# Kernel tuning notes

Hardware: AMD Instinct MI355X
Metric: run time of the kernel (lower is better)

## Reference

```python
import jax, jax.numpy as jnp
import numpy as np

BN_EPS = 1e-5

def conv_block(x, w, b, g, beta, m, v, a):
    # 1x1 conv (pointwise) + eval-mode BatchNorm2d + PReLU (single shared alpha)
    y = jnp.einsum('oc,bcft->boft', w, x) + b[None, :, None, None]
    scale = (g / jnp.sqrt(v + BN_EPS))[None, :, None, None]
    y = (y - m[None, :, None, None]) * scale + beta[None, :, None, None]
    return jnp.where(y >= 0, y, a * y)

def setup_inputs() -> dict:
    key = jax.random.key(0)
    ks = jax.random.split(key, 16)
    B, C, F, T = 4, 64, 128, 512
    d_c = C // 2
    inp = jax.random.normal(ks[0], (B, C, F, T), dtype=jnp.float32)
    # qkv projection Conv2Dblock params (1x1 conv c -> d_c)
    w1 = jax.random.normal(ks[1], (d_c, C), dtype=jnp.float32) * (1.0 / np.sqrt(C))
    b1 = jax.random.normal(ks[2], (d_c,), dtype=jnp.float32) * 0.01
    g1 = jnp.ones((d_c,), jnp.float32)
    be1 = jnp.zeros((d_c,), jnp.float32)
    m1 = jax.random.normal(ks[3], (d_c,), dtype=jnp.float32) * 0.01
    v1 = jax.random.uniform(ks[4], (d_c,), jnp.float32, 0.5, 1.5)
    a1 = jnp.asarray(0.25, jnp.float32)
    # output projection Conv2Dblock params (1x1 conv d_c -> c)
    wp = jax.random.normal(ks[5], (C, d_c), dtype=jnp.float32) * (1.0 / np.sqrt(d_c))
    bp = jax.random.normal(ks[6], (C,), dtype=jnp.float32) * 0.01
    g2 = jnp.ones((C,), jnp.float32)
    be2 = jnp.zeros((C,), jnp.float32)
    m2 = jax.random.normal(ks[7], (C,), dtype=jnp.float32) * 0.01
    v2 = jax.random.uniform(ks[8], (C,), jnp.float32, 0.5, 1.5)
    a2 = jnp.asarray(0.25, jnp.float32)
    return {"inp": inp, "w1": w1, "b1": b1, "g1": g1, "be1": be1, "m1": m1,
            "v1": v1, "a1": a1, "wp": wp, "bp": bp, "g2": g2, "be2": be2,
            "m2": m2, "v2": v2, "a2": a2}

def reference(inp, w1, b1, g1, be1, m1, v1, a1, wp, bp, g2, be2, m2, v2, a2):
    d_c = w1.shape[0]
    qkv = conv_block(inp, w1, b1, g1, be1, m1, v1, a1)           # [B, d_c, F, T]
    # per-frequency time attention scores, then recombine with values
    score = jnp.einsum('bcft,bcfy->bfty', qkv, qkv) / jnp.sqrt(jnp.asarray(d_c, qkv.dtype))
    score = jnp.einsum('bfty,bcfy->bcft', score, qkv)            # [B, d_c, F, T]
    # causal mask applied over the last two dims (F, T), as in the original
    Fd, Td = score.shape[-2], score.shape[-1]
    mask = (jnp.arange(Td)[None, :] - jnp.arange(Fd)[:, None]) >= (Td - Fd + 1)
    neg = -jnp.finfo(score.dtype).max
    score = jnp.where(mask[None, None, :, :], neg, score)
    score = jax.nn.softmax(score, axis=-1)
    score = conv_block(score, wp, bp, g2, be2, m2, v2, a2)       # [B, C, F, T]
    return score + inp
```

## Files before the change

kernel.cpp:

```cpp
#include <hip/hip_runtime.h>
#include <math.h>

#define Bv  4
#define Cv  64
#define DCv 32
#define Fv  128
#define Tv  512
#define FT  (Fv * 512)

__global__ __launch_bounds__(512)
void kprep(const float* __restrict__ w1, const float* __restrict__ b1,
           const float* __restrict__ g1, const float* __restrict__ be1,
           const float* __restrict__ m1, const float* __restrict__ v1,
           const float* __restrict__ wp, const float* __restrict__ bp,
           const float* __restrict__ g2, const float* __restrict__ be2,
           const float* __restrict__ m2, const float* __restrict__ v2,
           float* __restrict__ W1T, float* __restrict__ B1f,
           float* __restrict__ W2f, float* __restrict__ B2f)
{
    const int tid = threadIdx.x;
    #pragma unroll
    for (int i = 0; i < 4; ++i) {
        const int e = tid * 4 + i;
        const int c = e & 31, k = e >> 5;
        W1T[e] = w1[c * Cv + k] * (g1[c] * rsqrtf(v1[c] + 1e-5f));
    }
    {
        const int o = tid >> 3;
        const float s = g2[o] * rsqrtf(v2[o] + 1e-5f);
        float4 v = *(const float4*)&wp[tid * 4];
        v.x *= s; v.y *= s; v.z *= s; v.w *= s;
        *(float4*)&W2f[tid * 4] = v;
    }
    if (tid < DCv) {
        const float s = g1[tid] * rsqrtf(v1[tid] + 1e-5f);
        B1f[tid] = (b1[tid] - m1[tid]) * s + be1[tid];
    }
    if (tid < Cv) {
        const float s = g2[tid] * rsqrtf(v2[tid] + 1e-5f);
        B2f[tid] = (bp[tid] - m2[tid]) * s + be2[tid];
    }
}

__global__ __launch_bounds__(256, 4)
void kc1_conv(const float* __restrict__ inp,
              const float* __restrict__ W1T, const float* __restrict__ B1f,
              const float* __restrict__ a1,
              float* __restrict__ Qws)
{
    __shared__ __align__(16) float sW[Cv * DCv];
    __shared__ float sB[DCv];

    const int tid = threadIdx.x;
    const int bid = blockIdx.x;
    const int h   = bid & 1;
    const int bf  = bid >> 1;
    const int b   = bf >> 7;
    const int f   = bf & 127;

    {
        const int e = tid * 8;
        *(float4*)&sW[e]     = *(const float4*)&W1T[e];
        *(float4*)&sW[e + 4] = *(const float4*)&W1T[e + 4];
    }
    if (tid < DCv) sB[tid] = B1f[tid];
    const float alpha1 = a1[0];
    __syncthreads();

    const int w  = tid >> 6, l = tid & 63;
    const int tl = l & 15, cl = l >> 4;
    const int r0 = cl * 8;
    const int t0 = h * 256 + w * 64 + tl * 4;

    const float* px = inp + (size_t)(b * Cv) * FT + f * 512 + t0;

    float acc[32];
    #pragma unroll
    for (int i = 0; i < 32; ++i) acc[i] = 0.f;

    #pragma unroll 8
    for (int k = 0; k < Cv; ++k) {
        const float4 x   = *(const float4*)&px[(size_t)k * FT];
        const float4 a0  = *(const float4*)&sW[k * DCv + r0];
        const float4 a1v = *(const float4*)&sW[k * DCv + r0 + 4];
        acc[0*4+0] = fmaf(a0.x, x.x, acc[0*4+0]); acc[0*4+1] = fmaf(a0.x, x.y, acc[0*4+1]);
        acc[0*4+2] = fmaf(a0.x, x.z, acc[0*4+2]); acc[0*4+3] = fmaf(a0.x, x.w, acc[0*4+3]);
        acc[1*4+0] = fmaf(a0.y, x.x, acc[1*4+0]); acc[1*4+1] = fmaf(a0.y, x.y, acc[1*4+1]);
        acc[1*4+2] = fmaf(a0.y, x.z, acc[1*4+2]); acc[1*4+3] = fmaf(a0.y, x.w, acc[1*4+3]);
        acc[2*4+0] = fmaf(a0.z, x.x, acc[2*4+0]); acc[2*4+1] = fmaf(a0.z, x.y, acc[2*4+1]);
        acc[2*4+2] = fmaf(a0.z, x.z, acc[2*4+2]); acc[2*4+3] = fmaf(a0.z, x.w, acc[2*4+3]);
        acc[3*4+0] = fmaf(a0.w, x.x, acc[3*4+0]); acc[3*4+1] = fmaf(a0.w, x.y, acc[3*4+1]);
        acc[3*4+2] = fmaf(a0.w, x.z, acc[3*4+2]); acc[3*4+3] = fmaf(a0.w, x.w, acc[3*4+3]);
        acc[4*4+0] = fmaf(a1v.x, x.x, acc[4*4+0]); acc[4*4+1] = fmaf(a1v.x, x.y, acc[4*4+1]);
        acc[4*4+2] = fmaf(a1v.x, x.z, acc[4*4+2]); acc[4*4+3] = fmaf(a1v.x, x.w, acc[4*4+3]);
        acc[5*4+0] = fmaf(a1v.y, x.x, acc[5*4+0]); acc[5*4+1] = fmaf(a1v.y, x.y, acc[5*4+1]);
        acc[5*4+2] = fmaf(a1v.y, x.z, acc[5*4+2]); acc[5*4+3] = fmaf(a1v.y, x.w, acc[5*4+3]);
        acc[6*4+0] = fmaf(a1v.z, x.x, acc[6*4+0]); acc[6*4+1] = fmaf(a1v.z, x.y, acc[6*4+1]);
        acc[6*4+2] = fmaf(a1v.z, x.z, acc[6*4+2]); acc[6*4+3] = fmaf(a1v.z, x.w, acc[6*4+3]);
        acc[7*4+0] = fmaf(a1v.w, x.x, acc[7*4+0]); acc[7*4+1] = fmaf(a1v.w, x.y, acc[7*4+1]);
        acc[7*4+2] = fmaf(a1v.w, x.z, acc[7*4+2]); acc[7*4+3] = fmaf(a1v.w, x.w, acc[7*4+3]);
    }

    const float b0 = sB[r0+0], b1_ = sB[r0+1], b2 = sB[r0+2], b3 = sB[r0+3];
    const float b4 = sB[r0+4], b5  = sB[r0+5], b6 = sB[r0+6], b7 = sB[r0+7];
    #pragma unroll
    for (int j = 0; j < 4; ++j) {
        float z0 = acc[0*4+j] + b0, z1 = acc[1*4+j] + b1_;
        float z2 = acc[2*4+j] + b2, z3 = acc[3*4+j] + b3;
        float z4 = acc[4*4+j] + b4, z5 = acc[5*4+j] + b5;
        float z6 = acc[6*4+j] + b6, z7 = acc[7*4+j] + b7;
        z0 = z0 >= 0.f ? z0 : alpha1 * z0;  z1 = z1 >= 0.f ? z1 : alpha1 * z1;
        z2 = z2 >= 0.f ? z2 : alpha1 * z2;  z3 = z3 >= 0.f ? z3 : alpha1 * z3;
        z4 = z4 >= 0.f ? z4 : alpha1 * z4;  z5 = z5 >= 0.f ? z5 : alpha1 * z5;
        z6 = z6 >= 0.f ? z6 : alpha1 * z6;  z7 = z7 >= 0.f ? z7 : alpha1 * z7;
        float4 v0; v0.x = z0; v0.y = z1; v0.z = z2; v0.w = z3;
        float4 v1; v1.x = z4; v1.y = z5; v1.z = z6; v1.w = z7;
        float* qg = Qws + ((size_t)bf * Tv + t0 + j) * DCv + r0;
        *(float4*)&qg[0] = v0;
        *(float4*)&qg[4] = v1;
    }
}

__global__ __launch_bounds__(256)
void km_build(const float* __restrict__ Qws, float* __restrict__ Mfull)
{
    __shared__ __align__(16) float sP[4][1024];

    const int tid   = threadIdx.x;
    const int bf    = blockIdx.x;
    const int slice = tid >> 6;
    const int l     = tid & 63;
    const int c1b   = l >> 3;
    const int c2b   = l & 7;

    const float* qp = Qws + ((size_t)bf * Tv + slice * 128) * DCv;
    float4 r0 = {0,0,0,0}, r1 = {0,0,0,0}, r2 = {0,0,0,0}, r3 = {0,0,0,0};
    #pragma unroll 4
    for (int i = 0; i < 128; ++i) {
        const float4 qa = *(const float4*)&qp[i * 32 + c1b * 4];
        const float4 qb = *(const float4*)&qp[i * 32 + c2b * 4];
        r0.x = fmaf(qa.x, qb.x, r0.x); r0.y = fmaf(qa.x, qb.y, r0.y);
        r0.z = fmaf(qa.x, qb.z, r0.z); r0.w = fmaf(qa.x, qb.w, r0.w);
        r1.x = fmaf(qa.y, qb.x, r1.x); r1.y = fmaf(qa.y, qb.y, r1.y);
        r1.z = fmaf(qa.y, qb.z, r1.z); r1.w = fmaf(qa.y, qb.w, r1.w);
        r2.x = fmaf(qa.z, qb.x, r2.x); r2.y = fmaf(qa.z, qb.y, r2.y);
        r2.z = fmaf(qa.z, qb.z, r2.z); r2.w = fmaf(qa.z, qb.w, r2.w);
        r3.x = fmaf(qa.w, qb.x, r3.x); r3.y = fmaf(qa.w, qb.y, r3.y);
        r3.z = fmaf(qa.w, qb.z, r3.z); r3.w = fmaf(qa.w, qb.w, r3.w);
    }
    *(float4*)&sP[slice][(c1b * 4 + 0) * DCv + c2b * 4] = r0;
    *(float4*)&sP[slice][(c1b * 4 + 1) * DCv + c2b * 4] = r1;
    *(float4*)&sP[slice][(c1b * 4 + 2) * DCv + c2b * 4] = r2;
    *(float4*)&sP[slice][(c1b * 4 + 3) * DCv + c2b * 4] = r3;
    __syncthreads();

    const float INV = 0.17677669529663687f;
    float4 v0 = *(const float4*)&sP[0][tid * 4];
    float4 v1 = *(const float4*)&sP[1][tid * 4];
    float4 v2 = *(const float4*)&sP[2][tid * 4];
    float4 v3 = *(const float4*)&sP[3][tid * 4];
    float4 o;
    o.x = ((v0.x + v1.x) + (v2.x + v3.x)) * INV;
    o.y = ((v0.y + v1.y) + (v2.y + v3.y)) * INV;
    o.z = ((v0.z + v1.z) + (v2.z + v3.z)) * INV;
    o.w = ((v0.w + v1.w) + (v2.w + v3.w)) * INV;
    *(float4*)&Mfull[(size_t)bf * 1024 + tid * 4] = o;
}

#define GEMM_CC(ACC, cc, a)                                       \
    ACC[(cc)*4+0] = fmaf(a.x, x0.x, ACC[(cc)*4+0]);               \
    ACC[(cc)*4+0] = fmaf(a.y, x1.x, ACC[(cc)*4+0]);               \
    ACC[(cc)*4+0] = fmaf(a.z, x2.x, ACC[(cc)*4+0]);               \
    ACC[(cc)*4+0] = fmaf(a.w, x3.x, ACC[(cc)*4+0]);               \
    ACC[(cc)*4+1] = fmaf(a.x, x0.y, ACC[(cc)*4+1]);               \
    ACC[(cc)*4+1] = fmaf(a.y, x1.y, ACC[(cc)*4+1]);               \
    ACC[(cc)*4+1] = fmaf(a.z, x2.y, ACC[(cc)*4+1]);               \
    ACC[(cc)*4+1] = fmaf(a.w, x3.y, ACC[(cc)*4+1]);               \
    ACC[(cc)*4+2] = fmaf(a.x, x0.z, ACC[(cc)*4+2]);               \
    ACC[(cc)*4+2] = fmaf(a.y, x1.z, ACC[(cc)*4+2]);               \
    ACC[(cc)*4+2] = fmaf(a.z, x2.z, ACC[(cc)*4+2]);               \
    ACC[(cc)*4+2] = fmaf(a.w, x3.z, ACC[(cc)*4+2]);               \
    ACC[(cc)*4+3] = fmaf(a.x, x0.w, ACC[(cc)*4+3]);               \
    ACC[(cc)*4+3] = fmaf(a.y, x1.w, ACC[(cc)*4+3]);               \
    ACC[(cc)*4+3] = fmaf(a.z, x2.w, ACC[(cc)*4+3]);               \
    ACC[(cc)*4+3] = fmaf(a.w, x3.w, ACC[(cc)*4+3]);

__global__ __launch_bounds__(512, 2)
void kf_fused(const float* __restrict__ inp,
              const float* __restrict__ Qws, const float* __restrict__ Mfull,
              const float* __restrict__ W2f, const float* __restrict__ B2f,
              const float* __restrict__ a2,
              float* __restrict__ out)
{
    __shared__ __align__(16) float sX[DCv * Tv];
    __shared__ __align__(16) float sM[DCv * 36];
    __shared__ __align__(16) float sW[Cv * 36];
    __shared__ float sPart[8][DCv];
    __shared__ float sMx[DCv], sRZ[DCv];
    __shared__ float sB2[Cv];

    const int tid = threadIdx.x;
    const int bf  = blockIdx.x;
    const int b   = bf >> 7;
    const int f   = bf & 127;
    const int w   = tid >> 6;
    const int l   = tid & 63;
    const int tl  = l & 15;
    const int cl  = l >> 4;
    const int t0  = w * 64 + tl * 4;
    const int limit = f + (Tv - Fv + 1);
    const float alpha2 = a2[0];

    const float* qg = Qws + ((size_t)bf * Tv + tid) * DCv;
    float4 q0 = *(const float4*)&qg[0],  q1 = *(const float4*)&qg[4];
    float4 q2 = *(const float4*)&qg[8],  q3 = *(const float4*)&qg[12];
    float4 q4 = *(const float4*)&qg[16], q5 = *(const float4*)&qg[20];
    float4 q6 = *(const float4*)&qg[24], q7 = *(const float4*)&qg[28];

    if (tid < 256) {
        const int c = tid >> 3, k0 = (tid & 7) << 2;
        float4 v = *(const float4*)&Mfull[(size_t)bf * 1024 + tid * 4];
        *(float4*)&sM[c * 36 + k0] = v;
    }
    {
        const int c = tid >> 3, k0 = (tid & 7) << 2;
        float4 v = *(const float4*)&W2f[tid * 4];
        *(float4*)&sW[c * 36 + k0] = v;
    }
    if (tid < Cv) sB2[tid] = B2f[tid];

    {
        const int t = tid;
        sX[ 0*Tv+t]=q0.x; sX[ 1*Tv+t]=q0.y; sX[ 2*Tv+t]=q0.z; sX[ 3*Tv+t]=q0.w;
        sX[ 4*Tv+t]=q1.x; sX[ 5*Tv+t]=q1.y; sX[ 6*Tv+t]=q1.z; sX[ 7*Tv+t]=q1.w;
        sX[ 8*Tv+t]=q2.x; sX[ 9*Tv+t]=q2.y; sX[10*Tv+t]=q2.z; sX[11*Tv+t]=q2.w;
        sX[12*Tv+t]=q3.x; sX[13*Tv+t]=q3.y; sX[14*Tv+t]=q3.z; sX[15*Tv+t]=q3.w;
        sX[16*Tv+t]=q4.x; sX[17*Tv+t]=q4.y; sX[18*Tv+t]=q4.z; sX[19*Tv+t]=q4.w;
        sX[20*Tv+t]=q5.x; sX[21*Tv+t]=q5.y; sX[22*Tv+t]=q5.z; sX[23*Tv+t]=q5.w;
        sX[24*Tv+t]=q6.x; sX[25*Tv+t]=q6.y; sX[26*Tv+t]=q6.z; sX[27*Tv+t]=q6.w;
        sX[28*Tv+t]=q7.x; sX[29*Tv+t]=q7.y; sX[30*Tv+t]=q7.z; sX[31*Tv+t]=q7.w;
    }
    __syncthreads();

    float oA[16], oB[16];
    #pragma unroll
    for (int i = 0; i < 16; ++i) { oA[i] = 0.f; oB[i] = 0.f; }
    const int cA = cl * 4;
    const int cB = 16 + cl * 4;
    #pragma unroll
    for (int k0 = 0; k0 < 32; k0 += 4) {
        const float4 x0 = *(const float4*)&sX[(k0+0)*Tv + t0];
        const float4 x1 = *(const float4*)&sX[(k0+1)*Tv + t0];
        const float4 x2 = *(const float4*)&sX[(k0+2)*Tv + t0];
        const float4 x3 = *(const float4*)&sX[(k0+3)*Tv + t0];
        { const float4 a = *(const float4*)&sM[(cA+0)*36 + k0]; GEMM_CC(oA,0,a) }
        { const float4 a = *(const float4*)&sM[(cA+1)*36 + k0]; GEMM_CC(oA,1,a) }
        { const float4 a = *(const float4*)&sM[(cA+2)*36 + k0]; GEMM_CC(oA,2,a) }
        { const float4 a = *(const float4*)&sM[(cA+3)*36 + k0]; GEMM_CC(oA,3,a) }
        { const float4 a = *(const float4*)&sM[(cB+0)*36 + k0]; GEMM_CC(oB,0,a) }
        { const float4 a = *(const float4*)&sM[(cB+1)*36 + k0]; GEMM_CC(oB,1,a) }
        { const float4 a = *(const float4*)&sM[(cB+2)*36 + k0]; GEMM_CC(oB,2,a) }
        { const float4 a = *(const float4*)&sM[(cB+3)*36 + k0]; GEMM_CC(oB,3,a) }
    }

    #pragma unroll
    for (int jt = 0; jt < 4; ++jt) {
        if (t0 + jt >= limit) {
            #pragma unroll
            for (int cc = 0; cc < 4; ++cc) { oA[cc*4+jt] = -INFINITY; oB[cc*4+jt] = -INFINITY; }
        }
    }

    #pragma unroll
    for (int cc = 0; cc < 4; ++cc) {
        float mA = fmaxf(fmaxf(oA[cc*4+0], oA[cc*4+1]), fmaxf(oA[cc*4+2], oA[cc*4+3]));
        float mB = fmaxf(fmaxf(oB[cc*4+0], oB[cc*4+1]), fmaxf(oB[cc*4+2], oB[cc*4+3]));
        #pragma unroll
        for (int s = 1; s < 16; s <<= 1) {
            mA = fmaxf(mA, __shfl_xor(mA, s));
            mB = fmaxf(mB, __shfl_xor(mB, s));
        }
        if (tl == 0) { sPart[w][cA + cc] = mA; sPart[w][cB + cc] = mB; }
    }
    __syncthreads();
    if (tid < DCv) {
        float m = sPart[0][tid];
        #pragma unroll
        for (int ww = 1; ww < 8; ++ww) m = fmaxf(m, sPart[ww][tid]);
        sMx[tid] = m;
    }
    __syncthreads();

    #pragma unroll
    for (int cc = 0; cc < 4; ++cc) {
        const float mxA = sMx[cA + cc], mxB = sMx[cB + cc];
        float sA = 0.f, sB = 0.f;
        #pragma unroll
        for (int jt = 0; jt < 4; ++jt) {
            oA[cc*4+jt] = __expf(oA[cc*4+jt] - mxA); sA += oA[cc*4+jt];
            oB[cc*4+jt] = __expf(oB[cc*4+jt] - mxB); sB += oB[cc*4+jt];
        }
        #pragma unroll
        for (int s = 1; s < 16; s <<= 1) {
            sA += __shfl_xor(sA, s);
            sB += __shfl_xor(sB, s);
        }
        if (tl == 0) { sPart[w][cA + cc] = sA; sPart[w][cB + cc] = sB; }
    }
    __syncthreads();
    if (tid < DCv) {
        float z = 0.f;
        #pragma unroll
        for (int ww = 0; ww < 8; ++ww) z += sPart[ww][tid];
        sRZ[tid] = 1.f / z;
    }
    __syncthreads();

    #pragma unroll
    for (int cc = 0; cc < 4; ++cc) {
        const float rA = sRZ[cA + cc], rB = sRZ[cB + cc];
        float4 pA, pB;
        pA.x = oA[cc*4+0]*rA; pA.y = oA[cc*4+1]*rA; pA.z = oA[cc*4+2]*rA; pA.w = oA[cc*4+3]*rA;
        pB.x = oB[cc*4+0]*rB; pB.y = oB[cc*4+1]*rB; pB.z = oB[cc*4+2]*rB; pB.w = oB[cc*4+3]*rB;
        *(float4*)&sX[(cA + cc)*Tv + t0] = pA;
        *(float4*)&sX[(cB + cc)*Tv + t0] = pB;
    }
    __syncthreads();

    #pragma unroll 1
    for (int it = 0; it < 2; ++it) {
        const int oc0 = it * 32 + cl * 8;

        float acc[32];
        #pragma unroll
        for (int i = 0; i < 32; ++i) acc[i] = 0.f;

        #pragma unroll
        for (int k0 = 0; k0 < 32; k0 += 4) {
            const float4 x0 = *(const float4*)&sX[(k0+0)*Tv + t0];
            const float4 x1 = *(const float4*)&sX[(k0+1)*Tv + t0];
            const float4 x2 = *(const float4*)&sX[(k0+2)*Tv + t0];
            const float4 x3 = *(const float4*)&sX[(k0+3)*Tv + t0];
            { const float4 a = *(const float4*)&sW[(oc0+0)*36 + k0]; GEMM_CC(acc,0,a) }
            { const float4 a = *(const float4*)&sW[(oc0+1)*36 + k0]; GEMM_CC(acc,1,a) }
            { const float4 a = *(const float4*)&sW[(oc0+2)*36 + k0]; GEMM_CC(acc,2,a) }
            { const float4 a = *(const float4*)&sW[(oc0+3)*36 + k0]; GEMM_CC(acc,3,a) }
            { const float4 a = *(const float4*)&sW[(oc0+4)*36 + k0]; GEMM_CC(acc,4,a) }
            { const float4 a = *(const float4*)&sW[(oc0+5)*36 + k0]; GEMM_CC(acc,5,a) }
            { const float4 a = *(const float4*)&sW[(oc0+6)*36 + k0]; GEMM_CC(acc,6,a) }
            { const float4 a = *(const float4*)&sW[(oc0+7)*36 + k0]; GEMM_CC(acc,7,a) }
        }

        const float* rp = inp + ((size_t)(b * Cv + oc0) * Fv + f) * Tv + t0;
        float*       po = out + ((size_t)(b * Cv + oc0) * Fv + f) * Tv + t0;
        #pragma unroll
        for (int r = 0; r < 8; ++r) {
            const float4 rv = *(const float4*)&rp[(size_t)r * FT];
            const float bb = sB2[oc0 + r];
            float z0 = acc[r*4+0] + bb, z1 = acc[r*4+1] + bb;
            float z2 = acc[r*4+2] + bb, z3 = acc[r*4+3] + bb;
            z0 = z0 >= 0.f ? z0 : alpha2 * z0;
            z1 = z1 >= 0.f ? z1 : alpha2 * z1;
            z2 = z2 >= 0.f ? z2 : alpha2 * z2;
            z3 = z3 >= 0.f ? z3 : alpha2 * z3;
            float4 o4; o4.x = z0 + rv.x; o4.y = z1 + rv.y;
            o4.z = z2 + rv.z; o4.w = z3 + rv.w;
            *(float4*)&po[(size_t)r * FT] = o4;
        }
    }
}

extern "C" void kernel_launch(void* const* d_in, const int* in_sizes, int n_in,
                              void* d_out, int out_size, void* d_ws, size_t ws_size,
                              hipStream_t stream) {
    const float* inp = (const float*)d_in[0];
    const float* w1  = (const float*)d_in[1];
    const float* b1  = (const float*)d_in[2];
    const float* g1  = (const float*)d_in[3];
    const float* be1 = (const float*)d_in[4];
    const float* m1  = (const float*)d_in[5];
    const float* v1  = (const float*)d_in[6];
    const float* a1  = (const float*)d_in[7];
    const float* wp  = (const float*)d_in[8];
    const float* bp  = (const float*)d_in[9];
    const float* g2  = (const float*)d_in[10];
    const float* be2 = (const float*)d_in[11];
    const float* m2  = (const float*)d_in[12];
    const float* v2  = (const float*)d_in[13];
    const float* a2  = (const float*)d_in[14];

    float* Qws   = (float*)d_ws;
    float* Mfull = Qws   + (size_t)Bv * Fv * Tv * DCv;
    float* W1T   = Mfull + (size_t)512 * 1024;
    float* B1f   = W1T   + 2048;
    float* W2f   = B1f   + 32;
    float* B2f   = W2f   + 2048;

    kprep<<<dim3(1), dim3(512), 0, stream>>>(
        w1, b1, g1, be1, m1, v1, wp, bp, g2, be2, m2, v2, W1T, B1f, W2f, B2f);
    kc1_conv<<<dim3(Bv * Fv * 2), dim3(256), 0, stream>>>(inp, W1T, B1f, a1, Qws);
    km_build<<<dim3(Bv * Fv), dim3(256), 0, stream>>>(Qws, Mfull);
    kf_fused<<<dim3(Bv * Fv), dim3(512), 0, stream>>>(
        inp, Qws, Mfull, W2f, B2f, a2, (float*)d_out);
}
```

Baseline: 90.94 us.

## Read Q directly from global and stage softmax probs as bf16 in LDS

The first GEMM now loads Q rows straight from global memory instead of transposing them into a 64KB fp32 LDS tile. The softmax probabilities are stored to LDS as bf16 in a padded buffer of about 33KB, halving the LDS footprint and traffic for the second GEMM. The goal is to cut LDS usage so more blocks fit per CU, and to drop the transpose-store phase and its barrier. In exchange it adds bf16 rounding on the probabilities, so accuracy drops, and per-thread strided global loads for Q.

```diff
diff --git a/kernel.cpp b/kernel.cpp
--- a/kernel.cpp
+++ b/kernel.cpp
@@ -7,6 +7,17 @@
 #define Fv  128
 #define Tv  512
 #define FT  (Fv * 512)
+
+__device__ __forceinline__ unsigned f2bf(float x) {
+    unsigned u = __float_as_uint(x);
+    return (u + 0x7FFFu + ((u >> 16) & 1u)) >> 16;
+}
+__device__ __forceinline__ float bflo(unsigned u) { return __uint_as_float(u << 16); }
+__device__ __forceinline__ float bfhi(unsigned u) { return __uint_as_float(u & 0xFFFF0000u); }
+
+#define DOT4(ACC, A, X) \
+    ACC = fmaf(A.x, X.x, ACC); ACC = fmaf(A.y, X.y, ACC); \
+    ACC = fmaf(A.z, X.z, ACC); ACC = fmaf(A.w, X.w, ACC);
 
 __global__ __launch_bounds__(512)
 void kprep(const float* __restrict__ w1, const float* __restrict__ b1,
@@ -167,24 +178,6 @@
     *(float4*)&Mfull[(size_t)bf * 1024 + tid * 4] = o;
 }
 
-#define GEMM_CC(ACC, cc, a)                                       \
-    ACC[(cc)*4+0] = fmaf(a.x, x0.x, ACC[(cc)*4+0]);               \
-    ACC[(cc)*4+0] = fmaf(a.y, x1.x, ACC[(cc)*4+0]);               \
-    ACC[(cc)*4+0] = fmaf(a.z, x2.x, ACC[(cc)*4+0]);               \
-    ACC[(cc)*4+0] = fmaf(a.w, x3.x, ACC[(cc)*4+0]);               \
-    ACC[(cc)*4+1] = fmaf(a.x, x0.y, ACC[(cc)*4+1]);               \
-    ACC[(cc)*4+1] = fmaf(a.y, x1.y, ACC[(cc)*4+1]);               \
-    ACC[(cc)*4+1] = fmaf(a.z, x2.y, ACC[(cc)*4+1]);               \
-    ACC[(cc)*4+1] = fmaf(a.w, x3.y, ACC[(cc)*4+1]);               \
-    ACC[(cc)*4+2] = fmaf(a.x, x0.z, ACC[(cc)*4+2]);               \
-    ACC[(cc)*4+2] = fmaf(a.y, x1.z, ACC[(cc)*4+2]);               \
-    ACC[(cc)*4+2] = fmaf(a.z, x2.z, ACC[(cc)*4+2]);               \
-    ACC[(cc)*4+2] = fmaf(a.w, x3.z, ACC[(cc)*4+2]);               \
-    ACC[(cc)*4+3] = fmaf(a.x, x0.w, ACC[(cc)*4+3]);               \
-    ACC[(cc)*4+3] = fmaf(a.y, x1.w, ACC[(cc)*4+3]);               \
-    ACC[(cc)*4+3] = fmaf(a.z, x2.w, ACC[(cc)*4+3]);               \
-    ACC[(cc)*4+3] = fmaf(a.w, x3.w, ACC[(cc)*4+3]);
-
 __global__ __launch_bounds__(512, 2)
 void kf_fused(const float* __restrict__ inp,
               const float* __restrict__ Qws, const float* __restrict__ Mfull,
@@ -192,7 +185,7 @@
               const float* __restrict__ a2,
               float* __restrict__ out)
 {
-    __shared__ __align__(16) float sX[DCv * Tv];
+    __shared__ __align__(16) unsigned short sPb[DCv * 520];
     __shared__ __align__(16) float sM[DCv * 36];
     __shared__ __align__(16) float sW[Cv * 36];
     __shared__ float sPart[8][DCv];
@@ -211,12 +204,6 @@
     const int limit = f + (Tv - Fv + 1);
     const float alpha2 = a2[0];
 
-    const float* qg = Qws + ((size_t)bf * Tv + tid) * DCv;
-    float4 q0 = *(const float4*)&qg[0],  q1 = *(const float4*)&qg[4];
-    float4 q2 = *(const float4*)&qg[8],  q3 = *(const float4*)&qg[12];
-    float4 q4 = *(const float4*)&qg[16], q5 = *(const float4*)&qg[20];
-    float4 q6 = *(const float4*)&qg[24], q7 = *(const float4*)&qg[28];
-
     if (tid < 256) {
         const int c = tid >> 3, k0 = (tid & 7) << 2;
         float4 v = *(const float4*)&Mfull[(size_t)bf * 1024 + tid * 4];
@@ -228,20 +215,9 @@
         *(float4*)&sW[c * 36 + k0] = v;
     }
     if (tid < Cv) sB2[tid] = B2f[tid];
-
-    {
-        const int t = tid;
-        sX[ 0*Tv+t]=q0.x; sX[ 1*Tv+t]=q0.y; sX[ 2*Tv+t]=q0.z; sX[ 3*Tv+t]=q0.w;
-        sX[ 4*Tv+t]=q1.x; sX[ 5*Tv+t]=q1.y; sX[ 6*Tv+t]=q1.z; sX[ 7*Tv+t]=q1.w;
-        sX[ 8*Tv+t]=q2.x; sX[ 9*Tv+t]=q2.y; sX[10*Tv+t]=q2.z; sX[11*Tv+t]=q2.w;
-        sX[12*Tv+t]=q3.x; sX[13*Tv+t]=q3.y; sX[14*Tv+t]=q3.z; sX[15*Tv+t]=q3.w;
-        sX[16*Tv+t]=q4.x; sX[17*Tv+t]=q4.y; sX[18*Tv+t]=q4.z; sX[19*Tv+t]=q4.w;
-        sX[20*Tv+t]=q5.x; sX[21*Tv+t]=q5.y; sX[22*Tv+t]=q5.z; sX[23*Tv+t]=q5.w;
-        sX[24*Tv+t]=q6.x; sX[25*Tv+t]=q6.y; sX[26*Tv+t]=q6.z; sX[27*Tv+t]=q6.w;
-        sX[28*Tv+t]=q7.x; sX[29*Tv+t]=q7.y; sX[30*Tv+t]=q7.z; sX[31*Tv+t]=q7.w;
-    }
-    __syncthreads();
-
+    __syncthreads();
+
+    const float* Qb = Qws + (size_t)bf * Tv * DCv;
     float oA[16], oB[16];
     #pragma unroll
     for (int i = 0; i < 16; ++i) { oA[i] = 0.f; oB[i] = 0.f; }
@@ -249,18 +225,26 @@
     const int cB = 16 + cl * 4;
     #pragma unroll
     for (int k0 = 0; k0 < 32; k0 += 4) {
-        const float4 x0 = *(const float4*)&sX[(k0+0)*Tv + t0];
-        const float4 x1 = *(const float4*)&sX[(k0+1)*Tv + t0];
-        const float4 x2 = *(const float4*)&sX[(k0+2)*Tv + t0];
-        const float4 x3 = *(const float4*)&sX[(k0+3)*Tv + t0];
-        { const float4 a = *(const float4*)&sM[(cA+0)*36 + k0]; GEMM_CC(oA,0,a) }
-        { const float4 a = *(const float4*)&sM[(cA+1)*36 + k0]; GEMM_CC(oA,1,a) }
-        { const float4 a = *(const float4*)&sM[(cA+2)*36 + k0]; GEMM_CC(oA,2,a) }
-        { const float4 a = *(const float4*)&sM[(cA+3)*36 + k0]; GEMM_CC(oA,3,a) }
-        { const float4 a = *(const float4*)&sM[(cB+0)*36 + k0]; GEMM_CC(oB,0,a) }
-        { const float4 a = *(const float4*)&sM[(cB+1)*36 + k0]; GEMM_CC(oB,1,a) }
-        { const float4 a = *(const float4*)&sM[(cB+2)*36 + k0]; GEMM_CC(oB,2,a) }
-        { const float4 a = *(const float4*)&sM[(cB+3)*36 + k0]; GEMM_CC(oB,3,a) }
+        const float4 x0 = *(const float4*)&Qb[(t0+0) * DCv + k0];
+        const float4 x1 = *(const float4*)&Qb[(t0+1) * DCv + k0];
+        const float4 x2 = *(const float4*)&Qb[(t0+2) * DCv + k0];
+        const float4 x3 = *(const float4*)&Qb[(t0+3) * DCv + k0];
+        { const float4 a = *(const float4*)&sM[(cA+0)*36 + k0];
+          DOT4(oA[0],  a, x0) DOT4(oA[1],  a, x1) DOT4(oA[2],  a, x2) DOT4(oA[3],  a, x3) }
+        { const float4 a = *(const float4*)&sM[(cA+1)*36 + k0];
+          DOT4(oA[4],  a, x0) DOT4(oA[5],  a, x1) DOT4(oA[6],  a, x2) DOT4(oA[7],  a, x3) }
+        { const float4 a = *(const float4*)&sM[(cA+2)*36 + k0];
+          DOT4(oA[8],  a, x0) DOT4(oA[9],  a, x1) DOT4(oA[10], a, x2) DOT4(oA[11], a, x3) }
+        { const float4 a = *(const float4*)&sM[(cA+3)*36 + k0];
+          DOT4(oA[12], a, x0) DOT4(oA[13], a, x1) DOT4(oA[14], a, x2) DOT4(oA[15], a, x3) }
+        { const float4 a = *(const float4*)&sM[(cB+0)*36 + k0];
+          DOT4(oB[0],  a, x0) DOT4(oB[1],  a, x1) DOT4(oB[2],  a, x2) DOT4(oB[3],  a, x3) }
+        { const float4 a = *(const float4*)&sM[(cB+1)*36 + k0];
+          DOT4(oB[4],  a, x0) DOT4(oB[5],  a, x1) DOT4(oB[6],  a, x2) DOT4(oB[7],  a, x3) }
+        { const float4 a = *(const float4*)&sM[(cB+2)*36 + k0];
+          DOT4(oB[8],  a, x0) DOT4(oB[9],  a, x1) DOT4(oB[10], a, x2) DOT4(oB[11], a, x3) }
+        { const float4 a = *(const float4*)&sM[(cB+3)*36 + k0];
+          DOT4(oB[12], a, x0) DOT4(oB[13], a, x1) DOT4(oB[14], a, x2) DOT4(oB[15], a, x3) }
     }
 
     #pragma unroll
@@ -319,11 +303,13 @@
     #pragma unroll
     for (int cc = 0; cc < 4; ++cc) {
         const float rA = sRZ[cA + cc], rB = sRZ[cB + cc];
-        float4 pA, pB;
-        pA.x = oA[cc*4+0]*rA; pA.y = oA[cc*4+1]*rA; pA.z = oA[cc*4+2]*rA; pA.w = oA[cc*4+3]*rA;
-        pB.x = oB[cc*4+0]*rB; pB.y = oB[cc*4+1]*rB; pB.z = oB[cc*4+2]*rB; pB.w = oB[cc*4+3]*rB;
-        *(float4*)&sX[(cA + cc)*Tv + t0] = pA;
-        *(float4*)&sX[(cB + cc)*Tv + t0] = pB;
+        uint2 wA, wB;
+        wA.x = f2bf(oA[cc*4+0]*rA) | (f2bf(oA[cc*4+1]*rA) << 16);
+        wA.y = f2bf(oA[cc*4+2]*rA) | (f2bf(oA[cc*4+3]*rA) << 16);
+        wB.x = f2bf(oB[cc*4+0]*rB) | (f2bf(oB[cc*4+1]*rB) << 16);
+        wB.y = f2bf(oB[cc*4+2]*rB) | (f2bf(oB[cc*4+3]*rB) << 16);
+        *(uint2*)&sPb[(cA + cc) * 520 + t0] = wA;
+        *(uint2*)&sPb[(cB + cc) * 520 + t0] = wB;
     }
     __syncthreads();
 
@@ -337,18 +323,31 @@
 
         #pragma unroll
         for (int k0 = 0; k0 < 32; k0 += 4) {
-            const float4 x0 = *(const float4*)&sX[(k0+0)*Tv + t0];
-            const float4 x1 = *(const float4*)&sX[(k0+1)*Tv + t0];
-            const float4 x2 = *(const float4*)&sX[(k0+2)*Tv + t0];
-            const float4 x3 = *(const float4*)&sX[(k0+3)*Tv + t0];
-            { const float4 a = *(const float4*)&sW[(oc0+0)*36 + k0]; GEMM_CC(acc,0,a) }
-            { const float4 a = *(const float4*)&sW[(oc0+1)*36 + k0]; GEMM_CC(acc,1,a) }
-            { const float4 a = *(const float4*)&sW[(oc0+2)*36 + k0]; GEMM_CC(acc,2,a) }
-            { const float4 a = *(const float4*)&sW[(oc0+3)*36 + k0]; GEMM_CC(acc,3,a) }
-            { const float4 a = *(const float4*)&sW[(oc0+4)*36 + k0]; GEMM_CC(acc,4,a) }
-            { const float4 a = *(const float4*)&sW[(oc0+5)*36 + k0]; GEMM_CC(acc,5,a) }
-            { const float4 a = *(const float4*)&sW[(oc0+6)*36 + k0]; GEMM_CC(acc,6,a) }
-            { const float4 a = *(const float4*)&sW[(oc0+7)*36 + k0]; GEMM_CC(acc,7,a) }
+            const uint2 p0 = *(const uint2*)&sPb[(k0+0) * 520 + t0];
+            const uint2 p1 = *(const uint2*)&sPb[(k0+1) * 520 + t0];
+            const uint2 p2 = *(const uint2*)&sPb[(k0+2) * 520 + t0];
+            const uint2 p3 = *(const uint2*)&sPb[(k0+3) * 520 + t0];
+            float4 xt0, xt1, xt2, xt3;
+            xt0.x = bflo(p0.x); xt0.y = bflo(p1.x); xt0.z = bflo(p2.x); xt0.w = bflo(p3.x);
+            xt1.x = bfhi(p0.x); xt1.y = bfhi(p1.x); xt1.z = bfhi(p2.x); xt1.w = bfhi(p3.x);
+            xt2.x = bflo(p0.y); xt2.y = bflo(p1.y); xt2.z = bflo(p2.y); xt2.w = bflo(p3.y);
+            xt3.x = bfhi(p0.y); xt3.y = bfhi(p1.y); xt3.z = bfhi(p2.y); xt3.w = bfhi(p3.y);
+            { const float4 a = *(const float4*)&sW[(oc0+0)*36 + k0];
+              DOT4(acc[0],  a, xt0) DOT4(acc[1],  a, xt1) DOT4(acc[2],  a, xt2) DOT4(acc[3],  a, xt3) }
+            { const float4 a = *(const float4*)&sW[(oc0+1)*36 + k0];
+              DOT4(acc[4],  a, xt0) DOT4(acc[5],  a, xt1) DOT4(acc[6],  a, xt2) DOT4(acc[7],  a, xt3) }
+            { const float4 a = *(const float4*)&sW[(oc0+2)*36 + k0];
+              DOT4(acc[8],  a, xt0) DOT4(acc[9],  a, xt1) DOT4(acc[10], a, xt2) DOT4(acc[11], a, xt3) }
+            { const float4 a = *(const float4*)&sW[(oc0+3)*36 + k0];
+              DOT4(acc[12], a, xt0) DOT4(acc[13], a, xt1) DOT4(acc[14], a, xt2) DOT4(acc[15], a, xt3) }
+            { const float4 a = *(const float4*)&sW[(oc0+4)*36 + k0];
+              DOT4(acc[16], a, xt0) DOT4(acc[17], a, xt1) DOT4(acc[18], a, xt2) DOT4(acc[19], a, xt3) }
+            { const float4 a = *(const float4*)&sW[(oc0+5)*36 + k0];
+              DOT4(acc[20], a, xt0) DOT4(acc[21], a, xt1) DOT4(acc[22], a, xt2) DOT4(acc[23], a, xt3) }
+            { const float4 a = *(const float4*)&sW[(oc0+6)*36 + k0];
+              DOT4(acc[24], a, xt0) DOT4(acc[25], a, xt1) DOT4(acc[26], a, xt2) DOT4(acc[27], a, xt3) }
+            { const float4 a = *(const float4*)&sW[(oc0+7)*36 + k0];
+              DOT4(acc[28], a, xt0) DOT4(acc[29], a, xt1) DOT4(acc[30], a, xt2) DOT4(acc[31], a, xt3) }
         }
 
         const float* rp = inp + ((size_t)(b * Cv + oc0) * Fv + f) * Tv + t0;
```

New measurement: 96.12 us. 1.06x slower.
